# Kernel tuning notes

Hardware: AMD Instinct MI355X
Metric: run time of the kernel (lower is better)

## Reference

```python
import jax, jax.numpy as jnp
import numpy as np

NUM_UNFOLDS = 6
TAU = 1.0
ELAPSED = 1.0

def setup_inputs() -> dict:
    key = jax.random.key(0)
    k1, k2, k3, k4 = jax.random.split(key, 4)
    B, D_IN, UNITS = 32768, 256, 512
    inputs = jax.random.normal(k1, (B, D_IN), dtype=jnp.float32)
    hidden_state = jax.random.normal(k2, (B, UNITS), dtype=jnp.float32)
    # glorot-ish scaling for kernel, orthogonal-ish (scaled normal) for recurrent
    kernel = jax.random.normal(k3, (D_IN, UNITS), dtype=jnp.float32) * (1.0 / np.sqrt(D_IN))
    recurrent_kernel = jax.random.normal(k4, (UNITS, UNITS), dtype=jnp.float32) * (1.0 / np.sqrt(UNITS))
    bias = jnp.zeros((UNITS,), dtype=jnp.float32)
    scale = jnp.ones((UNITS,), dtype=jnp.float32)
    return {"inputs": inputs, "hidden_state": hidden_state, "kernel": kernel,
            "recurrent_kernel": recurrent_kernel, "bias": bias, "scale": scale}

def _dfdt(x, h, kernel, recurrent_kernel, bias, scale):
    # dh = scale * tanh(x@K + h@R + b) - tau*h
    pre = x @ kernel + h @ recurrent_kernel + bias
    dh_in = scale * jnp.tanh(pre)
    return dh_in - h * TAU

def _rk4_step(x, h, dt, kernel, recurrent_kernel, bias, scale):
    k1 = _dfdt(x, h, kernel, recurrent_kernel, bias, scale)
    k2 = _dfdt(x, h + k1 * (dt * 0.5), kernel, recurrent_kernel, bias, scale)
    k3 = _dfdt(x, h + k2 * (dt * 0.5), kernel, recurrent_kernel, bias, scale)
    k4 = _dfdt(x, h + k3 * dt, kernel, recurrent_kernel, bias, scale)
    return h + dt * (k1 + 2.0 * k2 + 2.0 * k3 + k4) / 6.0

def reference(inputs, hidden_state, kernel, recurrent_kernel, bias, scale):
    dt = ELAPSED / NUM_UNFOLDS
    def body(h, _):
        return _rk4_step(inputs, h, dt, kernel, recurrent_kernel, bias, scale), None
    h, _ = jax.lax.scan(body, hidden_state, None, length=NUM_UNFOLDS)
    return h
```

## Files before the change

### kernel.cpp

```cpp
#include <hip/hip_runtime.h>

typedef unsigned int u32;
typedef unsigned short u16;
typedef __bf16 bf16x8 __attribute__((ext_vector_type(8)));
typedef float f32x16 __attribute__((ext_vector_type(16)));
typedef float f32x4v __attribute__((ext_vector_type(4)));
typedef u32 u32x4 __attribute__((ext_vector_type(4)));
typedef u32 u32x2 __attribute__((ext_vector_type(2)));

#define BATCH    32768
#define DIN      256
#define UNITS    512
#define BM       64
#define NTHREADS 1024
#define NSTEP    6
#define DT       (1.0f/6.0f)
#define SMEM_BYTES (65536 + 65536 + 32768)

__device__ __forceinline__ u16 f2bf(float f) {
  return __builtin_bit_cast(u16, (__bf16)f);
}
__device__ __forceinline__ float bf2f(u16 b) {
  return __builtin_bit_cast(float, (u32)b << 16);
}
__device__ __forceinline__ u32 pk2(float a, float b) {
  return (u32)f2bf(a) | ((u32)f2bf(b) << 16);
}
__device__ __forceinline__ float fast_tanh(float x) {
  float t = fminf(fmaxf(x * 2.885390082f, -60.f), 60.f);
  float a = __builtin_amdgcn_exp2f(t);
  return (a - 1.f) * __builtin_amdgcn_rcpf(a + 1.f);
}

__global__ void pack_weights(const float* __restrict__ Km, const float* __restrict__ Rm,
                             u16* __restrict__ Kp, u16* __restrict__ Rp) {
  int c = blockIdx.x * 256 + threadIdx.x;
  if (c < 32768) {
    int n = c & 511, g = c >> 9;
    u32x4 p;
#pragma unroll
    for (int i = 0; i < 4; ++i) {
      u16 lo = f2bf(Rm[(g * 8 + 2 * i) * 512 + n]);
      u16 hh = f2bf(Rm[(g * 8 + 2 * i + 1) * 512 + n]);
      p[i] = (u32)lo | ((u32)hh << 16);
    }
    ((u32x4*)Rp)[c] = p;
  } else {
    int c2 = c - 32768;
    int n = c2 & 511, g = c2 >> 9;
    u32x4 p;
#pragma unroll
    for (int i = 0; i < 4; ++i) {
      u16 lo = f2bf(Km[(g * 8 + 2 * i) * 512 + n]);
      u16 hh = f2bf(Km[(g * 8 + 2 * i + 1) * 512 + n]);
      p[i] = (u32)lo | ((u32)hh << 16);
    }
    ((u32x4*)Kp)[c2] = p;
  }
}

__global__ __launch_bounds__(NTHREADS, 4)
void ctrnn_fused(const float* __restrict__ X, const float* __restrict__ H0,
                 const u16* __restrict__ Kp, const u16* __restrict__ Rp,
                 const float* __restrict__ bias, const float* __restrict__ scale,
                 float* __restrict__ out) {
  extern __shared__ char smem[];
  char* heL  = smem;
  float* h1L = (float*)(smem + 65536);
  u32* xkbL1 = (u32*)(smem + 131072);

  const int tid  = threadIdx.x;
  const int lane = tid & 63;
  const int wv   = tid >> 6;
  const int ln   = lane & 31, hi = lane >> 5;
  const long r0  = (long)blockIdx.x * BM;

  const int jc  = wv * 32 + ln;
  const int swA = (ln & 7) << 4;

  {
    const f32x4v* X4 = (const f32x4v*)(X + r0 * DIN);
#pragma unroll
    for (int i = 0; i < 4; ++i) {
      int flat = i * NTHREADS + tid;
      int m = flat >> 6, c4 = flat & 63;
      f32x4v v = X4[m * 64 + c4];
      u32x2 p;
      p.x = pk2(v.x, v.y);
      p.y = pk2(v.z, v.w);
      *(u32x2*)(heL + m * 512 + ((c4 * 8) ^ ((m & 7) << 4))) = p;
    }
  }

  const float scl = scale[jc];

  float h0[16];
#pragma unroll
  for (int r = 0; r < 16; ++r) {
    int m = (r & 3) + ((r >> 2) << 3) + hi * 4;
    h0[r] = H0[(r0 + m) * UNITS + jc];
    h1L[r * NTHREADS + tid] = H0[(r0 + m + 32) * UNITS + jc];
  }

  __syncthreads();

  {
    f32x16 pre0, pre1;
    {
      float b = bias[jc];
#pragma unroll
      for (int r = 0; r < 16; ++r) { pre0[r] = b; pre1[r] = b; }
    }
    const u32x4* Kp4 = (const u32x4*)Kp;
#pragma unroll 2
    for (int kb = 0; kb < 16; ++kb) {
      bf16x8 a0 = __builtin_bit_cast(bf16x8,
          *(const u32x4*)(heL + ln * 512        + (((kb * 32) | (hi * 16)) ^ swA)));
      bf16x8 a1 = __builtin_bit_cast(bf16x8,
          *(const u32x4*)(heL + (32 + ln) * 512 + (((kb * 32) | (hi * 16)) ^ swA)));
      bf16x8 bb = __builtin_bit_cast(bf16x8, Kp4[(kb * 2 + hi) * 512 + jc]);
      pre0 = __builtin_amdgcn_mfma_f32_32x32x16_bf16(a0, bb, pre0, 0, 0, 0);
      pre1 = __builtin_amdgcn_mfma_f32_32x32x16_bf16(a1, bb, pre1, 0, 0, 0);
    }
    u32 xkbP0t[8];
#pragma unroll
    for (int i = 0; i < 8; ++i) {
      xkbP0t[i] = pk2(pre0[2 * i], pre0[2 * i + 1]);
      xkbL1[i * NTHREADS + tid] = pk2(pre1[2 * i], pre1[2 * i + 1]);
    }
#pragma unroll
    for (int i = 0; i < 8; ++i) ((u32*)&smem[0])[0];
    __syncthreads();

#pragma unroll
    for (int r = 0; r < 16; ++r) {
      int m = (r & 3) + ((r >> 2) << 3) + hi * 4;
      *(u16*)(heL + m * 1024        + ((jc * 2) ^ ((m & 7) << 4)))        = f2bf(h0[r]);
      int m1 = m + 32;
      *(u16*)(heL + m1 * 1024       + ((jc * 2) ^ ((m1 & 7) << 4)))       = f2bf(h1L[r * NTHREADS + tid]);
    }
    __syncthreads();

    const u32x4* Rp4 = (const u32x4*)Rp;
    u32 accP0[8], accP1[8];
    u32 xkbP0[8];
#pragma unroll
    for (int i = 0; i < 8; ++i) xkbP0[i] = xkbP0t[i];

#pragma unroll 1
    for (int it = 0; it < NSTEP * 4; ++it) {
      const int ev = it & 3;
      const float wk = (ev == 1 || ev == 2) ? 2.f : 1.f;
      const float ce = (ev < 2) ? (DT * 0.5f) : DT;
      const bool ev0 = (ev == 0), ev3 = (ev == 3);
      const bool last = (it == NSTEP * 4 - 1);

      f32x16 p0, p1;
#pragma unroll
      for (int i = 0; i < 8; ++i) {
        u32 q0 = xkbP0[i];
        u32 q1 = xkbL1[i * NTHREADS + tid];
        p0[2 * i]     = bf2f((u16)(q0 & 0xffffu));
        p0[2 * i + 1] = bf2f((u16)(q0 >> 16));
        p1[2 * i]     = bf2f((u16)(q1 & 0xffffu));
        p1[2 * i + 1] = bf2f((u16)(q1 >> 16));
      }
#pragma unroll 2
      for (int kb = 0; kb < 32; ++kb) {
        bf16x8 a0 = __builtin_bit_cast(bf16x8,
            *(const u32x4*)(heL + ln * 1024        + (((kb * 32) | (hi * 16)) ^ swA)));
        bf16x8 a1 = __builtin_bit_cast(bf16x8,
            *(const u32x4*)(heL + (32 + ln) * 1024 + (((kb * 32) | (hi * 16)) ^ swA)));
        bf16x8 bb = __builtin_bit_cast(bf16x8, Rp4[(kb * 2 + hi) * 512 + jc]);
        p0 = __builtin_amdgcn_mfma_f32_32x32x16_bf16(a0, bb, p0, 0, 0, 0);
        p1 = __builtin_amdgcn_mfma_f32_32x32x16_bf16(a1, bb, p1, 0, 0, 0);
      }

#pragma unroll
      for (int rp = 0; rp < 8; ++rp) {
        int m0 = ((2 * rp) & 3) + (((2 * rp) >> 2) << 3) + hi * 4;
        int m1 = ((2 * rp + 1) & 3) + (((2 * rp + 1) >> 2) << 3) + hi * 4;
        float he0 = bf2f(*(const u16*)(heL + m0 * 1024 + ((jc * 2) ^ ((m0 & 7) << 4))));
        float he1 = bf2f(*(const u16*)(heL + m1 * 1024 + ((jc * 2) ^ ((m1 & 7) << 4))));
        float k0 = scl * fast_tanh(p0[2 * rp])     - he0;
        float k1 = scl * fast_tanh(p0[2 * rp + 1]) - he1;
        float a0 = (ev0 ? 0.f : bf2f((u16)(accP0[rp] & 0xffffu))) + wk * k0;
        float a1 = (ev0 ? 0.f : bf2f((u16)(accP0[rp] >> 16)))     + wk * k1;
        if (ev3) {
          h0[2 * rp]     += (DT / 6.f) * a0;
          h0[2 * rp + 1] += (DT / 6.f) * a1;
        } else {
          accP0[rp] = pk2(a0, a1);
        }
        p0[2 * rp] = k0; p0[2 * rp + 1] = k1;
      }
#pragma unroll
      for (int rp = 0; rp < 8; ++rp) {
        int m0 = ((2 * rp) & 3) + (((2 * rp) >> 2) << 3) + hi * 4 + 32;
        int m1 = ((2 * rp + 1) & 3) + (((2 * rp + 1) >> 2) << 3) + hi * 4 + 32;
        float he0 = bf2f(*(const u16*)(heL + m0 * 1024 + ((jc * 2) ^ ((m0 & 7) << 4))));
        float he1 = bf2f(*(const u16*)(heL + m1 * 1024 + ((jc * 2) ^ ((m1 & 7) << 4))));
        float k0 = scl * fast_tanh(p1[2 * rp])     - he0;
        float k1 = scl * fast_tanh(p1[2 * rp + 1]) - he1;
        float a0 = (ev0 ? 0.f : bf2f((u16)(accP1[rp] & 0xffffu))) + wk * k0;
        float a1 = (ev0 ? 0.f : bf2f((u16)(accP1[rp] >> 16)))     + wk * k1;
        if (ev3) {
          float hv0 = h1L[(2 * rp) * NTHREADS + tid]     + (DT / 6.f) * a0;
          float hv1 = h1L[(2 * rp + 1) * NTHREADS + tid] + (DT / 6.f) * a1;
          h1L[(2 * rp) * NTHREADS + tid]     = hv0;
          h1L[(2 * rp + 1) * NTHREADS + tid] = hv1;
        } else {
          accP1[rp] = pk2(a0, a1);
        }
        p1[2 * rp] = k0; p1[2 * rp + 1] = k1;
      }
      __syncthreads();

      if (!last) {
#pragma unroll
        for (int r = 0; r < 16; ++r) {
          int m = (r & 3) + ((r >> 2) << 3) + hi * 4;
          float v0 = ev3 ? h0[r] : h0[r] + ce * p0[r];
          *(u16*)(heL + m * 1024 + ((jc * 2) ^ ((m & 7) << 4))) = f2bf(v0);
          int m1 = m + 32;
          float hv = h1L[r * NTHREADS + tid];
          float v1 = ev3 ? hv : hv + ce * p1[r];
          *(u16*)(heL + m1 * 1024 + ((jc * 2) ^ ((m1 & 7) << 4))) = f2bf(v1);
        }
        __syncthreads();
      }
    }
  }

#pragma unroll
  for (int r = 0; r < 16; ++r) {
    int m = (r & 3) + ((r >> 2) << 3) + hi * 4;
    out[(r0 + m) * UNITS + jc]      = h0[r];
    out[(r0 + m + 32) * UNITS + jc] = h1L[r * NTHREADS + tid];
  }
}

extern "C" void kernel_launch(void* const* d_in, const int* in_sizes, int n_in,
                              void* d_out, int out_size, void* d_ws, size_t ws_size,
                              hipStream_t stream) {
  const float* X     = (const float*)d_in[0];
  const float* H0    = (const float*)d_in[1];
  const float* Km    = (const float*)d_in[2];
  const float* Rm    = (const float*)d_in[3];
  const float* bias  = (const float*)d_in[4];
  const float* scale = (const float*)d_in[5];
  float* out = (float*)d_out;

  u16* Rp = (u16*)d_ws;
  u16* Kp = Rp + UNITS * UNITS;

  (void)hipFuncSetAttribute((const void*)ctrnn_fused,
                            hipFuncAttributeMaxDynamicSharedMemorySize, SMEM_BYTES);

  pack_weights<<<192, 256, 0, stream>>>(Km, Rm, Kp, Rp);
  ctrnn_fused<<<BATCH / BM, NTHREADS, SMEM_BYTES, stream>>>(X, H0, Kp, Rp, bias, scale, out);
}
```

Baseline: 677.5 us.

## Fold tanh scale into weights and specialize RK4 stages at compile time

The tanh exponent constant is folded into the packed K and R weights and the bias, so the per-element multiply before exp2 goes away. Each of the four RK4 stages is specialised at compile time through a templated lambda, removing runtime stage branches. The MFMA loops are fully unrolled, LDS addresses come from precomputed bases, and the bf16 unpacking uses shift and mask. Scaling the weights before rounding to bf16 changes rounding slightly, and full unrolling raises code size and register pressure.

Measured after the change: 2.516 ms. +271.4%, slower.

```diff
diff --git a/kernel.cpp b/kernel.cpp
--- a/kernel.cpp
+++ b/kernel.cpp
@@ -15,7 +15,10 @@
 #define NTHREADS 1024
 #define NSTEP    6
 #define DT       (1.0f/6.0f)
+#define TANH_C   2.885390082f
 #define SMEM_BYTES (65536 + 65536 + 32768)
+
+template <int E> struct IC { static constexpr int value = E; };
 
 __device__ __forceinline__ u16 f2bf(float f) {
   return __builtin_bit_cast(u16, (__bf16)f);
@@ -26,9 +29,9 @@
 __device__ __forceinline__ u32 pk2(float a, float b) {
   return (u32)f2bf(a) | ((u32)f2bf(b) << 16);
 }
-__device__ __forceinline__ float fast_tanh(float x) {
-  float t = fminf(fmaxf(x * 2.885390082f, -60.f), 60.f);
-  float a = __builtin_amdgcn_exp2f(t);
+__device__ __forceinline__ float tanh_pre(float t) {
+  float tt = fminf(fmaxf(t, -60.f), 60.f);
+  float a = __builtin_amdgcn_exp2f(tt);
   return (a - 1.f) * __builtin_amdgcn_rcpf(a + 1.f);
 }
 
@@ -40,8 +43,8 @@
     u32x4 p;
 #pragma unroll
     for (int i = 0; i < 4; ++i) {
-      u16 lo = f2bf(Rm[(g * 8 + 2 * i) * 512 + n]);
-      u16 hh = f2bf(Rm[(g * 8 + 2 * i + 1) * 512 + n]);
+      u16 lo = f2bf(Rm[(g * 8 + 2 * i) * 512 + n] * TANH_C);
+      u16 hh = f2bf(Rm[(g * 8 + 2 * i + 1) * 512 + n] * TANH_C);
       p[i] = (u32)lo | ((u32)hh << 16);
     }
     ((u32x4*)Rp)[c] = p;
@@ -51,8 +54,8 @@
     u32x4 p;
 #pragma unroll
     for (int i = 0; i < 4; ++i) {
-      u16 lo = f2bf(Km[(g * 8 + 2 * i) * 512 + n]);
-      u16 hh = f2bf(Km[(g * 8 + 2 * i + 1) * 512 + n]);
+      u16 lo = f2bf(Km[(g * 8 + 2 * i) * 512 + n] * TANH_C);
+      u16 hh = f2bf(Km[(g * 8 + 2 * i + 1) * 512 + n] * TANH_C);
       p[i] = (u32)lo | ((u32)hh << 16);
     }
     ((u32x4*)Kp)[c2] = p;
@@ -104,15 +107,23 @@
 
   __syncthreads();
 
+  int aBase[4], hB[4];
+#pragma unroll
+  for (int v = 0; v < 4; ++v) {
+    aBase[v] = ln * 1024 + (((v * 32) | (hi * 16)) ^ swA);
+    hB[v] = ((jc * 2) ^ ((hi * 4 + v) << 4)) + (hi * 4 + v) * 1024;
+  }
+
+  u32 xkbP0[8];
   {
     f32x16 pre0, pre1;
     {
-      float b = bias[jc];
+      float b = bias[jc] * TANH_C;
 #pragma unroll
       for (int r = 0; r < 16; ++r) { pre0[r] = b; pre1[r] = b; }
     }
     const u32x4* Kp4 = (const u32x4*)Kp;
-#pragma unroll 2
+#pragma unroll
     for (int kb = 0; kb < 16; ++kb) {
       bf16x8 a0 = __builtin_bit_cast(bf16x8,
           *(const u32x4*)(heL + ln * 512        + (((kb * 32) | (hi * 16)) ^ swA)));
@@ -122,114 +133,122 @@
       pre0 = __builtin_amdgcn_mfma_f32_32x32x16_bf16(a0, bb, pre0, 0, 0, 0);
       pre1 = __builtin_amdgcn_mfma_f32_32x32x16_bf16(a1, bb, pre1, 0, 0, 0);
     }
-    u32 xkbP0t[8];
 #pragma unroll
     for (int i = 0; i < 8; ++i) {
-      xkbP0t[i] = pk2(pre0[2 * i], pre0[2 * i + 1]);
+      xkbP0[i] = pk2(pre0[2 * i], pre0[2 * i + 1]);
       xkbL1[i * NTHREADS + tid] = pk2(pre1[2 * i], pre1[2 * i + 1]);
     }
-#pragma unroll
-    for (int i = 0; i < 8; ++i) ((u32*)&smem[0])[0];
+  }
+  __syncthreads();
+
+#pragma unroll
+  for (int r = 0; r < 16; ++r) {
+    int off = hB[r & 3] + (r >> 2) * 8192;
+    *(u16*)(heL + off)         = f2bf(h0[r]);
+    *(u16*)(heL + off + 32768) = f2bf(h1L[r * NTHREADS + tid]);
+  }
+  __syncthreads();
+
+  const u32x4* Rp4 = (const u32x4*)Rp;
+  u32 accP0[8], accP1[8];
+
+  auto evalfn = [&](auto EVC, bool skipw) {
+    constexpr int ev = decltype(EVC)::value;
+    constexpr float wk  = (ev == 1 || ev == 2) ? 2.f : 1.f;
+    constexpr float ce  = (ev < 2) ? (DT * 0.5f) : DT;
+    constexpr float dt6 = DT / 6.f;
+
+    f32x16 p0, p1;
+#pragma unroll
+    for (int i = 0; i < 8; ++i) {
+      u32 q0 = xkbP0[i];
+      u32 q1 = xkbL1[i * NTHREADS + tid];
+      p0[2 * i]     = __builtin_bit_cast(float, q0 << 16);
+      p0[2 * i + 1] = __builtin_bit_cast(float, q0 & 0xffff0000u);
+      p1[2 * i]     = __builtin_bit_cast(float, q1 << 16);
+      p1[2 * i + 1] = __builtin_bit_cast(float, q1 & 0xffff0000u);
+    }
+#pragma unroll
+    for (int kb = 0; kb < 32; ++kb) {
+      bf16x8 a0 = __builtin_bit_cast(bf16x8,
+          *(const u32x4*)(heL + aBase[kb & 3] + (kb >> 2) * 128));
+      bf16x8 a1 = __builtin_bit_cast(bf16x8,
+          *(const u32x4*)(heL + aBase[kb & 3] + (kb >> 2) * 128 + 32768));
+      bf16x8 bb = __builtin_bit_cast(bf16x8, Rp4[(kb * 2 + hi) * 512 + jc]);
+      p0 = __builtin_amdgcn_mfma_f32_32x32x16_bf16(a0, bb, p0, 0, 0, 0);
+      p1 = __builtin_amdgcn_mfma_f32_32x32x16_bf16(a1, bb, p1, 0, 0, 0);
+    }
+
+#pragma unroll
+    for (int rp = 0; rp < 8; ++rp) {
+      const int off = hB[(2 * rp) & 3] + (rp >> 1) * 8192;
+      const int off1 = hB[((2 * rp) & 3) + 1] + (rp >> 1) * 8192;
+      float he0 = bf2f(*(const u16*)(heL + off));
+      float he1 = bf2f(*(const u16*)(heL + off1));
+      float k0 = scl * tanh_pre(p0[2 * rp])     - he0;
+      float k1 = scl * tanh_pre(p0[2 * rp + 1]) - he1;
+      float a0, a1;
+      if constexpr (ev == 0) { a0 = k0; a1 = k1; }
+      else {
+        a0 = bf2f((u16)(accP0[rp] & 0xffffu)) + wk * k0;
+        a1 = bf2f((u16)(accP0[rp] >> 16))     + wk * k1;
+      }
+      if constexpr (ev == 3) {
+        h0[2 * rp]     += dt6 * a0;
+        h0[2 * rp + 1] += dt6 * a1;
+        p0[2 * rp] = h0[2 * rp]; p0[2 * rp + 1] = h0[2 * rp + 1];
+      } else {
+        accP0[rp] = pk2(a0, a1);
+        p0[2 * rp]     = h0[2 * rp]     + ce * k0;
+        p0[2 * rp + 1] = h0[2 * rp + 1] + ce * k1;
+      }
+    }
+#pragma unroll
+    for (int rp = 0; rp < 8; ++rp) {
+      const int off = hB[(2 * rp) & 3] + (rp >> 1) * 8192 + 32768;
+      const int off1 = hB[((2 * rp) & 3) + 1] + (rp >> 1) * 8192 + 32768;
+      float he0 = bf2f(*(const u16*)(heL + off));
+      float he1 = bf2f(*(const u16*)(heL + off1));
+      float k0 = scl * tanh_pre(p1[2 * rp])     - he0;
+      float k1 = scl * tanh_pre(p1[2 * rp + 1]) - he1;
+      float a0, a1;
+      if constexpr (ev == 0) { a0 = k0; a1 = k1; }
+      else {
+        a0 = bf2f((u16)(accP1[rp] & 0xffffu)) + wk * k0;
+        a1 = bf2f((u16)(accP1[rp] >> 16))     + wk * k1;
+      }
+      float hv0 = h1L[(2 * rp) * NTHREADS + tid];
+      float hv1 = h1L[(2 * rp + 1) * NTHREADS + tid];
+      if constexpr (ev == 3) {
+        hv0 += dt6 * a0; hv1 += dt6 * a1;
+        h1L[(2 * rp) * NTHREADS + tid]     = hv0;
+        h1L[(2 * rp + 1) * NTHREADS + tid] = hv1;
+        p1[2 * rp] = hv0; p1[2 * rp + 1] = hv1;
+      } else {
+        accP1[rp] = pk2(a0, a1);
+        p1[2 * rp]     = hv0 + ce * k0;
+        p1[2 * rp + 1] = hv1 + ce * k1;
+      }
+    }
     __syncthreads();
 
-#pragma unroll
-    for (int r = 0; r < 16; ++r) {
-      int m = (r & 3) + ((r >> 2) << 3) + hi * 4;
-      *(u16*)(heL + m * 1024        + ((jc * 2) ^ ((m & 7) << 4)))        = f2bf(h0[r]);
-      int m1 = m + 32;
-      *(u16*)(heL + m1 * 1024       + ((jc * 2) ^ ((m1 & 7) << 4)))       = f2bf(h1L[r * NTHREADS + tid]);
-    }
-    __syncthreads();
-
-    const u32x4* Rp4 = (const u32x4*)Rp;
-    u32 accP0[8], accP1[8];
-    u32 xkbP0[8];
-#pragma unroll
-    for (int i = 0; i < 8; ++i) xkbP0[i] = xkbP0t[i];
+    if (!skipw) {
+#pragma unroll
+      for (int r = 0; r < 16; ++r) {
+        int off = hB[r & 3] + (r >> 2) * 8192;
+        *(u16*)(heL + off)         = f2bf(p0[r]);
+        *(u16*)(heL + off + 32768) = f2bf(p1[r]);
+      }
+      __syncthreads();
+    }
+  };
 
 #pragma unroll 1
-    for (int it = 0; it < NSTEP * 4; ++it) {
-      const int ev = it & 3;
-      const float wk = (ev == 1 || ev == 2) ? 2.f : 1.f;
-      const float ce = (ev < 2) ? (DT * 0.5f) : DT;
-      const bool ev0 = (ev == 0), ev3 = (ev == 3);
-      const bool last = (it == NSTEP * 4 - 1);
-
-      f32x16 p0, p1;
-#pragma unroll
-      for (int i = 0; i < 8; ++i) {
-        u32 q0 = xkbP0[i];
-        u32 q1 = xkbL1[i * NTHREADS + tid];
-        p0[2 * i]     = bf2f((u16)(q0 & 0xffffu));
-        p0[2 * i + 1] = bf2f((u16)(q0 >> 16));
-        p1[2 * i]     = bf2f((u16)(q1 & 0xffffu));
-        p1[2 * i + 1] = bf2f((u16)(q1 >> 16));
-      }
-#pragma unroll 2
-      for (int kb = 0; kb < 32; ++kb) {
-        bf16x8 a0 = __builtin_bit_cast(bf16x8,
-            *(const u32x4*)(heL + ln * 1024        + (((kb * 32) | (hi * 16)) ^ swA)));
-        bf16x8 a1 = __builtin_bit_cast(bf16x8,
-            *(const u32x4*)(heL + (32 + ln) * 1024 + (((kb * 32) | (hi * 16)) ^ swA)));
-        bf16x8 bb = __builtin_bit_cast(bf16x8, Rp4[(kb * 2 + hi) * 512 + jc]);
-        p0 = __builtin_amdgcn_mfma_f32_32x32x16_bf16(a0, bb, p0, 0, 0, 0);
-        p1 = __builtin_amdgcn_mfma_f32_32x32x16_bf16(a1, bb, p1, 0, 0, 0);
-      }
-
-#pragma unroll
-      for (int rp = 0; rp < 8; ++rp) {
-        int m0 = ((2 * rp) & 3) + (((2 * rp) >> 2) << 3) + hi * 4;
-        int m1 = ((2 * rp + 1) & 3) + (((2 * rp + 1) >> 2) << 3) + hi * 4;
-        float he0 = bf2f(*(const u16*)(heL + m0 * 1024 + ((jc * 2) ^ ((m0 & 7) << 4))));
-        float he1 = bf2f(*(const u16*)(heL + m1 * 1024 + ((jc * 2) ^ ((m1 & 7) << 4))));
-        float k0 = scl * fast_tanh(p0[2 * rp])     - he0;
-        float k1 = scl * fast_tanh(p0[2 * rp + 1]) - he1;
-        float a0 = (ev0 ? 0.f : bf2f((u16)(accP0[rp] & 0xffffu))) + wk * k0;
-        float a1 = (ev0 ? 0.f : bf2f((u16)(accP0[rp] >> 16)))     + wk * k1;
-        if (ev3) {
-          h0[2 * rp]     += (DT / 6.f) * a0;
-          h0[2 * rp + 1] += (DT / 6.f) * a1;
-        } else {
-          accP0[rp] = pk2(a0, a1);
-        }
-        p0[2 * rp] = k0; p0[2 * rp + 1] = k1;
-      }
-#pragma unroll
-      for (int rp = 0; rp < 8; ++rp) {
-        int m0 = ((2 * rp) & 3) + (((2 * rp) >> 2) << 3) + hi * 4 + 32;
-        int m1 = ((2 * rp + 1) & 3) + (((2 * rp + 1) >> 2) << 3) + hi * 4 + 32;
-        float he0 = bf2f(*(const u16*)(heL + m0 * 1024 + ((jc * 2) ^ ((m0 & 7) << 4))));
-        float he1 = bf2f(*(const u16*)(heL + m1 * 1024 + ((jc * 2) ^ ((m1 & 7) << 4))));
-        float k0 = scl * fast_tanh(p1[2 * rp])     - he0;
-        float k1 = scl * fast_tanh(p1[2 * rp + 1]) - he1;
-        float a0 = (ev0 ? 0.f : bf2f((u16)(accP1[rp] & 0xffffu))) + wk * k0;
-        float a1 = (ev0 ? 0.f : bf2f((u16)(accP1[rp] >> 16)))     + wk * k1;
-        if (ev3) {
-          float hv0 = h1L[(2 * rp) * NTHREADS + tid]     + (DT / 6.f) * a0;
-          float hv1 = h1L[(2 * rp + 1) * NTHREADS + tid] + (DT / 6.f) * a1;
-          h1L[(2 * rp) * NTHREADS + tid]     = hv0;
-          h1L[(2 * rp + 1) * NTHREADS + tid] = hv1;
-        } else {
-          accP1[rp] = pk2(a0, a1);
-        }
-        p1[2 * rp] = k0; p1[2 * rp + 1] = k1;
-      }
-      __syncthreads();
-
-      if (!last) {
-#pragma unroll
-        for (int r = 0; r < 16; ++r) {
-          int m = (r & 3) + ((r >> 2) << 3) + hi * 4;
-          float v0 = ev3 ? h0[r] : h0[r] + ce * p0[r];
-          *(u16*)(heL + m * 1024 + ((jc * 2) ^ ((m & 7) << 4))) = f2bf(v0);
-          int m1 = m + 32;
-          float hv = h1L[r * NTHREADS + tid];
-          float v1 = ev3 ? hv : hv + ce * p1[r];
-          *(u16*)(heL + m1 * 1024 + ((jc * 2) ^ ((m1 & 7) << 4))) = f2bf(v1);
-        }
-        __syncthreads();
-      }
-    }
+  for (int step = 0; step < NSTEP; ++step) {
+    evalfn(IC<0>{}, false);
+    evalfn(IC<1>{}, false);
+    evalfn(IC<2>{}, false);
+    evalfn(IC<3>{}, step == NSTEP - 1);
   }
 
 #pragma unroll
```
